# Kernel optimization log

Measured on AMD Instinct MI355X. Metric: run time of the kernel, lower is better.

Reference implementation:

```python
import jax, jax.numpy as jnp
import numpy as np

N_NODES = 100000
N_EDGES = 1600000
NODE_F = 128
EDGE_F = 64
OUT = 32
NEG_SLOPE = 0.01  # torch nn.LeakyReLU default


def setup_inputs() -> dict:
    key = jax.random.key(0)
    ks = jax.random.split(key, 7)
    h = jax.random.normal(ks[0], (N_NODES, NODE_F), dtype=jnp.float32)
    edge_feat = jax.random.normal(ks[1], (N_EDGES, EDGE_F), dtype=jnp.float32)
    src = jax.random.randint(ks[2], (N_EDGES,), 0, N_NODES)
    dst = jax.random.randint(ks[3], (N_EDGES,), 0, N_NODES)
    W_node = jax.random.normal(ks[4], (NODE_F, OUT), dtype=jnp.float32) * 0.05
    W_edge = jax.random.normal(ks[5], (EDGE_F, OUT), dtype=jnp.float32) * 0.05
    attn_w = jax.random.normal(ks[6], (3 * OUT,), dtype=jnp.float32) * 0.05
    return {"h": h, "edge_feat": edge_feat, "src": src, "dst": dst,
            "W_node": W_node, "W_edge": W_edge, "attn_w": attn_w}


def reference(h, edge_feat, src, dst, W_node, W_edge, attn_w):
    # Project node and edge features (bias-free linears).
    z = h @ W_node                      # [N, OUT]
    ez = edge_feat @ W_edge             # [E, OUT]

    # attn_fc on cat(src_z, dst_z, edge_z): split weight vector to avoid
    # materializing the [E, 3*OUT] concat.
    a_src, a_dst, a_edge = attn_w[:OUT], attn_w[OUT:2 * OUT], attn_w[2 * OUT:]
    zs = z[src]                         # [E, OUT] gather
    logits = jax.nn.leaky_relu(
        zs @ a_src + z[dst] @ a_dst + ez @ a_edge, NEG_SLOPE)  # [E]

    # Per-destination (segment) softmax over incoming edges.
    seg_max = jax.ops.segment_max(logits, dst, num_segments=N_NODES)
    seg_max = jnp.where(jnp.isfinite(seg_max), seg_max, 0.0)  # empty segments
    e = jnp.exp(logits - seg_max[dst])                          # [E]
    denom = jax.ops.segment_sum(e, dst, num_segments=N_NODES)  # [N]

    # Weighted sum of src z vectors per destination.
    num = jax.ops.segment_sum(e[:, None] * zs, dst, num_segments=N_NODES)
    u = num / jnp.maximum(denom, 1e-20)[:, None]                # [N, OUT]
    return u
```

## Files before the change

### kernel.cpp

```cpp
#include <hip/hip_runtime.h>
#include <hip/hip_bf16.h>

#define N_NODES 100000
#define N_EDGES 1600000
#define NODE_F 128
#define EDGE_F 64
#define OUT_F 32
#define NEG_SLOPE 0.01f

__global__ void k_edge_w(const float* __restrict__ W_edge,
                         const float* __restrict__ attn_w,
                         float* __restrict__ w_e) {
    int j = threadIdx.x;
    float acc = 0.f;
#pragma unroll
    for (int k = 0; k < OUT_F; ++k)
        acc += W_edge[j * OUT_F + k] * attn_w[2 * OUT_F + k];
    w_e[j] = acc;
}

__global__ void k_node_proj(const float* __restrict__ h,
                            const float* __restrict__ W_node,
                            const float* __restrict__ attn_w,
                            float* __restrict__ z,
                            float* __restrict__ s_src,
                            float* __restrict__ s_dst) {
    __shared__ float Ws[NODE_F * OUT_F];
    for (int i = threadIdx.x; i < NODE_F * OUT_F; i += 256)
        Ws[i] = W_node[i];
    __syncthreads();

    int node = blockIdx.x * 8 + (threadIdx.x >> 5);
    int o = threadIdx.x & 31;
    if (node >= N_NODES) return;

    const float* hrow = h + (size_t)node * NODE_F;
    float acc = 0.f;
#pragma unroll 8
    for (int j = 0; j < NODE_F; ++j)
        acc += hrow[j] * Ws[j * OUT_F + o];

    z[(size_t)node * OUT_F + o] = acc;

    float ps = acc * attn_w[o];
    float pd = acc * attn_w[OUT_F + o];
#pragma unroll
    for (int m = 16; m >= 1; m >>= 1) {
        ps += __shfl_xor(ps, m);
        pd += __shfl_xor(pd, m);
    }
    if (o == 0) {
        s_src[node] = ps;
        s_dst[node] = pd;
    }
}

__global__ void k_edge_dot(const float* __restrict__ edge_feat,
                           const int* __restrict__ dst,
                           const float* __restrict__ w_e,
                           float* __restrict__ g,
                           int* __restrict__ deg) {
    __shared__ float we_s[EDGE_F];
    if (threadIdx.x < EDGE_F) we_s[threadIdx.x] = w_e[threadIdx.x];
    __syncthreads();

    int t = blockIdx.x * 256 + threadIdx.x;
    int e = t >> 2;
    int sub = t & 3;
    if (e >= N_EDGES) return;

    const float4* row = (const float4*)(edge_feat + (size_t)e * EDGE_F);
    float acc = 0.f;
#pragma unroll
    for (int i = 0; i < 4; ++i) {
        int fi = sub + i * 4;
        float4 v = row[fi];
        int b = fi * 4;
        acc += v.x * we_s[b] + v.y * we_s[b + 1] + v.z * we_s[b + 2] + v.w * we_s[b + 3];
    }
    acc += __shfl_xor(acc, 1);
    acc += __shfl_xor(acc, 2);

    if (sub == 0) {
        g[e] = acc;
        atomicAdd(deg + dst[e], 1);
    }
}

__global__ void k_scan_block(const int* __restrict__ deg,
                             int* __restrict__ offs,
                             int* __restrict__ bsum) {
    __shared__ int wsum[4];
    int i = blockIdx.x * 256 + threadIdx.x;
    int lane = threadIdx.x & 63;
    int wid = threadIdx.x >> 6;
    int v = (i < N_NODES) ? deg[i] : 0;
    int x = v;
#pragma unroll
    for (int d = 1; d < 64; d <<= 1) {
        int y = __shfl_up(x, d);
        if (lane >= d) x += y;
    }
    if (lane == 63) wsum[wid] = x;
    __syncthreads();
    int add = 0;
    for (int w = 0; w < wid; ++w) add += wsum[w];
    int incl = x + add;
    if (i < N_NODES) offs[i] = incl - v;
    if (threadIdx.x == 255) bsum[blockIdx.x] = incl;
}

__global__ void k_scan_bsums(int* __restrict__ bsum, int nb) {
    __shared__ int wsum[8];
    int t = threadIdx.x;
    int lane = t & 63;
    int wid = t >> 6;
    int v = (t < nb) ? bsum[t] : 0;
    int x = v;
#pragma unroll
    for (int d = 1; d < 64; d <<= 1) {
        int y = __shfl_up(x, d);
        if (lane >= d) x += y;
    }
    if (lane == 63) wsum[wid] = x;
    __syncthreads();
    int add = 0;
    for (int w = 0; w < wid; ++w) add += wsum[w];
    int incl = x + add;
    if (t < nb) bsum[t] = incl - v;
}

__global__ void k_scan_add(int* __restrict__ offs,
                           const int* __restrict__ bsum,
                           int* __restrict__ cursor) {
    int i = blockIdx.x * 256 + threadIdx.x;
    if (i < N_NODES) {
        int o = offs[i] + bsum[blockIdx.x];
        offs[i] = o;
        cursor[i] = o;
    }
}

__global__ void k_scatter(const int* __restrict__ src,
                          const int* __restrict__ dst,
                          const float* __restrict__ g,
                          const float* __restrict__ s_src,
                          const float* __restrict__ s_dst,
                          int* __restrict__ cursor,
                          int2* __restrict__ perm) {
    int e = blockIdx.x * 256 + threadIdx.x;
    if (e >= N_EDGES) return;
    int s = src[e], d = dst[e];
    float logit = s_src[s] + s_dst[d] + g[e];
    logit = logit > 0.f ? logit : NEG_SLOPE * logit;
    float ev = __expf(logit);
    int pos = atomicAdd(cursor + d, 1);
    perm[pos] = make_int2(s, __float_as_int(ev));
}

__global__ void k_node_aggr(const int* __restrict__ offs,
                            const int* __restrict__ cursor,
                            const int2* __restrict__ perm,
                            const float* __restrict__ z,
                            float* __restrict__ out) {
    int node = blockIdx.x * 8 + (threadIdx.x >> 5);
    int k = threadIdx.x & 31;
    if (node >= N_NODES) return;

    int start = offs[node];
    int end = cursor[node];

    float acc = 0.f, den_local = 0.f;
    for (int base = start; base < end; base += 32) {
        int idx = base + k;
        int cnt = min(32, end - base);
        float ev = 0.f;
        int sp = 0;
        if (idx < end) {
            int2 pr = perm[idx];
            sp = pr.x;
            ev = __int_as_float(pr.y);
        }
        den_local += ev;
        int j = 0;
        for (; j + 4 <= cnt; j += 4) {
            float e0 = __shfl(ev, j, 32), e1 = __shfl(ev, j + 1, 32);
            float e2 = __shfl(ev, j + 2, 32), e3 = __shfl(ev, j + 3, 32);
            int s0 = __shfl(sp, j, 32), s1 = __shfl(sp, j + 1, 32);
            int s2 = __shfl(sp, j + 2, 32), s3 = __shfl(sp, j + 3, 32);
            float z0 = z[(size_t)s0 * OUT_F + k];
            float z1 = z[(size_t)s1 * OUT_F + k];
            float z2 = z[(size_t)s2 * OUT_F + k];
            float z3 = z[(size_t)s3 * OUT_F + k];
            acc += e0 * z0;
            acc += e1 * z1;
            acc += e2 * z2;
            acc += e3 * z3;
        }
        for (; j < cnt; ++j) {
            float evj = __shfl(ev, j, 32);
            int sj = __shfl(sp, j, 32);
            acc += evj * z[(size_t)sj * OUT_F + k];
        }
    }

    float den = den_local;
#pragma unroll
    for (int msk = 16; msk >= 1; msk >>= 1)
        den += __shfl_xor(den, msk, 32);

    out[(size_t)node * OUT_F + k] =
        (end > start) ? acc / fmaxf(den, 1e-20f) : 0.f;
}

extern "C" void kernel_launch(void* const* d_in, const int* in_sizes, int n_in,
                              void* d_out, int out_size, void* d_ws, size_t ws_size,
                              hipStream_t stream) {
    const float* h         = (const float*)d_in[0];
    const float* edge_feat = (const float*)d_in[1];
    const int*   src       = (const int*)d_in[2];
    const int*   dst       = (const int*)d_in[3];
    const float* W_node    = (const float*)d_in[4];
    const float* W_edge    = (const float*)d_in[5];
    const float* attn_w    = (const float*)d_in[6];
    float* out = (float*)d_out;

    char* ws = (char*)d_ws;
    size_t off = 0;
    auto alloc = [&](size_t bytes) {
        void* p = ws + off;
        off += (bytes + 255) & ~(size_t)255;
        return p;
    };
    float* z        = (float*)alloc((size_t)N_NODES * OUT_F * sizeof(float));
    float* s_src    = (float*)alloc((size_t)N_NODES * sizeof(float));
    float* s_dst    = (float*)alloc((size_t)N_NODES * sizeof(float));
    float* w_e      = (float*)alloc(EDGE_F * sizeof(float));
    float* g        = (float*)alloc((size_t)N_EDGES * sizeof(float));
    int*   deg      = (int*)alloc((size_t)N_NODES * sizeof(int));
    int*   offs     = (int*)alloc((size_t)N_NODES * sizeof(int));
    int*   cursor   = (int*)alloc((size_t)N_NODES * sizeof(int));
    int*   bsum     = (int*)alloc(1024 * sizeof(int));
    int2*  perm     = (int2*)alloc((size_t)N_EDGES * sizeof(int2));

    const int NB = (N_NODES + 255) / 256;

    hipMemsetAsync(deg, 0, (size_t)N_NODES * sizeof(int), stream);

    k_edge_w<<<1, 64, 0, stream>>>(W_edge, attn_w, w_e);
    k_node_proj<<<(N_NODES + 7) / 8, 256, 0, stream>>>(h, W_node, attn_w, z, s_src, s_dst);

    {
        int total = N_EDGES * 4;
        k_edge_dot<<<(total + 255) / 256, 256, 0, stream>>>(edge_feat, dst, w_e, g, deg);
    }
    k_scan_block<<<NB, 256, 0, stream>>>(deg, offs, bsum);
    k_scan_bsums<<<1, 512, 0, stream>>>(bsum, NB);
    k_scan_add<<<NB, 256, 0, stream>>>(offs, bsum, cursor);

    k_scatter<<<(N_EDGES + 255) / 256, 256, 0, stream>>>(
        src, dst, g, s_src, s_dst, cursor, perm);

    k_node_aggr<<<(N_NODES + 7) / 8, 256, 0, stream>>>(
        offs, cursor, perm, z, out);
}
```

Measured before the change: 288.2 us.

## Edge-tiled aggregation with LDS atomics, bf16 node projections, fused edge weight

Replaces the per-node warp aggregation with edge-tiled blocks of 256 sorted edges. Each block accumulates into LDS with atomics, writes nodes fully contained in its tile directly, and sends partial sums for boundary nodes to global atomic buffers; a finalize kernel then writes those boundary nodes. The projected z is stored as bf16 to halve gather traffic, and the edge-weight precompute is folded into k_edge_dot to remove one launch. The goal is to balance load across skewed degrees, at the cost of wider perm records (int4), extra memset, many atomics and reduced precision in z.

```diff
diff --git a/kernel.cpp b/kernel.cpp
--- a/kernel.cpp
+++ b/kernel.cpp
@@ -7,22 +7,22 @@
 #define EDGE_F 64
 #define OUT_F 32
 #define NEG_SLOPE 0.01f
-
-__global__ void k_edge_w(const float* __restrict__ W_edge,
-                         const float* __restrict__ attn_w,
-                         float* __restrict__ w_e) {
-    int j = threadIdx.x;
-    float acc = 0.f;
-#pragma unroll
-    for (int k = 0; k < OUT_F; ++k)
-        acc += W_edge[j * OUT_F + k] * attn_w[2 * OUT_F + k];
-    w_e[j] = acc;
+#define E_TILE 256
+#define SPAN_CAP 288
+
+__device__ __forceinline__ unsigned short f2bf(float f) {
+    unsigned u = __float_as_uint(f);
+    unsigned r = u + 0x7fffu + ((u >> 16) & 1u);
+    return (unsigned short)(r >> 16);
+}
+__device__ __forceinline__ float bf2f(unsigned short b) {
+    return __uint_as_float((unsigned)b << 16);
 }
 
 __global__ void k_node_proj(const float* __restrict__ h,
                             const float* __restrict__ W_node,
                             const float* __restrict__ attn_w,
-                            float* __restrict__ z,
+                            unsigned short* __restrict__ zb,
                             float* __restrict__ s_src,
                             float* __restrict__ s_dst) {
     __shared__ float Ws[NODE_F * OUT_F];
@@ -40,7 +40,7 @@
     for (int j = 0; j < NODE_F; ++j)
         acc += hrow[j] * Ws[j * OUT_F + o];
 
-    z[(size_t)node * OUT_F + o] = acc;
+    zb[(size_t)node * OUT_F + o] = f2bf(acc);
 
     float ps = acc * attn_w[o];
     float pd = acc * attn_w[OUT_F + o];
@@ -57,11 +57,18 @@
 
 __global__ void k_edge_dot(const float* __restrict__ edge_feat,
                            const int* __restrict__ dst,
-                           const float* __restrict__ w_e,
+                           const float* __restrict__ W_edge,
+                           const float* __restrict__ attn_w,
                            float* __restrict__ g,
                            int* __restrict__ deg) {
     __shared__ float we_s[EDGE_F];
-    if (threadIdx.x < EDGE_F) we_s[threadIdx.x] = w_e[threadIdx.x];
+    if (threadIdx.x < EDGE_F) {
+        float a = 0.f;
+#pragma unroll
+        for (int kk = 0; kk < OUT_F; ++kk)
+            a += W_edge[threadIdx.x * OUT_F + kk] * attn_w[2 * OUT_F + kk];
+        we_s[threadIdx.x] = a;
+    }
     __syncthreads();
 
     int t = blockIdx.x * 256 + threadIdx.x;
@@ -147,7 +154,7 @@
                           const float* __restrict__ s_src,
                           const float* __restrict__ s_dst,
                           int* __restrict__ cursor,
-                          int2* __restrict__ perm) {
+                          int4* __restrict__ perm4) {
     int e = blockIdx.x * 256 + threadIdx.x;
     if (e >= N_EDGES) return;
     int s = src[e], d = dst[e];
@@ -155,62 +162,96 @@
     logit = logit > 0.f ? logit : NEG_SLOPE * logit;
     float ev = __expf(logit);
     int pos = atomicAdd(cursor + d, 1);
-    perm[pos] = make_int2(s, __float_as_int(ev));
-}
-
-__global__ void k_node_aggr(const int* __restrict__ offs,
-                            const int* __restrict__ cursor,
-                            const int2* __restrict__ perm,
-                            const float* __restrict__ z,
-                            float* __restrict__ out) {
+    perm4[pos] = make_int4(s, __float_as_int(ev), d, 0);
+}
+
+__global__ __launch_bounds__(256) void k_aggr_seg(
+    const int4* __restrict__ perm4,
+    const unsigned short* __restrict__ zb,
+    const int* __restrict__ offs,
+    const int* __restrict__ endp,
+    float* __restrict__ gnum,
+    float* __restrict__ gden,
+    float* __restrict__ out) {
+    __shared__ float lds_num[SPAN_CAP * OUT_F];
+    __shared__ float lds_den[SPAN_CAP];
+    for (int i = threadIdx.x; i < SPAN_CAP * OUT_F; i += 256) lds_num[i] = 0.f;
+    for (int i = threadIdx.x; i < SPAN_CAP; i += 256) lds_den[i] = 0.f;
+    __syncthreads();
+
+    int e0 = blockIdx.x * E_TILE;
+    int n0 = perm4[e0].z;
+    int grp = threadIdx.x >> 5;
+    int k = threadIdx.x & 31;
+    int ebase = e0 + grp * 32;
+
+#pragma unroll 2
+    for (int j = 0; j < 32; j += 4) {
+        int4 pa = perm4[ebase + j + 0];
+        int4 pb = perm4[ebase + j + 1];
+        int4 pc = perm4[ebase + j + 2];
+        int4 pd = perm4[ebase + j + 3];
+        float za = bf2f(zb[(size_t)pa.x * OUT_F + k]);
+        float zv = bf2f(zb[(size_t)pb.x * OUT_F + k]);
+        float zc = bf2f(zb[(size_t)pc.x * OUT_F + k]);
+        float zd = bf2f(zb[(size_t)pd.x * OUT_F + k]);
+        float ea = __int_as_float(pa.y);
+        float eb = __int_as_float(pb.y);
+        float ec = __int_as_float(pc.y);
+        float ed = __int_as_float(pd.y);
+        int la = pa.z - n0, lb = pb.z - n0, lc = pc.z - n0, ld = pd.z - n0;
+
+        if (la < SPAN_CAP) { atomicAdd(&lds_num[la * OUT_F + k], ea * za); if (k == 0) atomicAdd(&lds_den[la], ea); }
+        else { atomicAdd(&gnum[(size_t)pa.z * OUT_F + k], ea * za); if (k == 0) atomicAdd(&gden[pa.z], ea); }
+        if (lb < SPAN_CAP) { atomicAdd(&lds_num[lb * OUT_F + k], eb * zv); if (k == 0) atomicAdd(&lds_den[lb], eb); }
+        else { atomicAdd(&gnum[(size_t)pb.z * OUT_F + k], eb * zv); if (k == 0) atomicAdd(&gden[pb.z], eb); }
+        if (lc < SPAN_CAP) { atomicAdd(&lds_num[lc * OUT_F + k], ec * zc); if (k == 0) atomicAdd(&lds_den[lc], ec); }
+        else { atomicAdd(&gnum[(size_t)pc.z * OUT_F + k], ec * zc); if (k == 0) atomicAdd(&gden[pc.z], ec); }
+        if (ld < SPAN_CAP) { atomicAdd(&lds_num[ld * OUT_F + k], ed * zd); if (k == 0) atomicAdd(&lds_den[ld], ed); }
+        else { atomicAdd(&gnum[(size_t)pd.z * OUT_F + k], ed * zd); if (k == 0) atomicAdd(&gden[pd.z], ed); }
+    }
+    __syncthreads();
+
+    int n_last = perm4[e0 + E_TILE - 1].z;
+    for (int nid = n0 + grp; nid <= n_last; nid += 8) {
+        int li = nid - n0;
+        if (li >= SPAN_CAP) break;
+        float den = lds_den[li];
+        if (den == 0.f) continue;
+        float nm = lds_num[li * OUT_F + k];
+        int st = offs[nid], en = endp[nid];
+        if (st >= e0 && en <= e0 + E_TILE) {
+            out[(size_t)nid * OUT_F + k] = nm / fmaxf(den, 1e-20f);
+        } else {
+            atomicAdd(&gnum[(size_t)nid * OUT_F + k], nm);
+            if (k == 0) atomicAdd(&gden[nid], den);
+        }
+    }
+}
+
+__global__ void k_finalize(const int* __restrict__ offs,
+                           const int* __restrict__ endp,
+                           const int4* __restrict__ perm4,
+                           const float* __restrict__ gnum,
+                           const float* __restrict__ gden,
+                           float* __restrict__ out) {
     int node = blockIdx.x * 8 + (threadIdx.x >> 5);
     int k = threadIdx.x & 31;
     if (node >= N_NODES) return;
-
-    int start = offs[node];
-    int end = cursor[node];
-
-    float acc = 0.f, den_local = 0.f;
-    for (int base = start; base < end; base += 32) {
-        int idx = base + k;
-        int cnt = min(32, end - base);
-        float ev = 0.f;
-        int sp = 0;
-        if (idx < end) {
-            int2 pr = perm[idx];
-            sp = pr.x;
-            ev = __int_as_float(pr.y);
-        }
-        den_local += ev;
-        int j = 0;
-        for (; j + 4 <= cnt; j += 4) {
-            float e0 = __shfl(ev, j, 32), e1 = __shfl(ev, j + 1, 32);
-            float e2 = __shfl(ev, j + 2, 32), e3 = __shfl(ev, j + 3, 32);
-            int s0 = __shfl(sp, j, 32), s1 = __shfl(sp, j + 1, 32);
-            int s2 = __shfl(sp, j + 2, 32), s3 = __shfl(sp, j + 3, 32);
-            float z0 = z[(size_t)s0 * OUT_F + k];
-            float z1 = z[(size_t)s1 * OUT_F + k];
-            float z2 = z[(size_t)s2 * OUT_F + k];
-            float z3 = z[(size_t)s3 * OUT_F + k];
-            acc += e0 * z0;
-            acc += e1 * z1;
-            acc += e2 * z2;
-            acc += e3 * z3;
-        }
-        for (; j < cnt; ++j) {
-            float evj = __shfl(ev, j, 32);
-            int sj = __shfl(sp, j, 32);
-            acc += evj * z[(size_t)sj * OUT_F + k];
-        }
-    }
-
-    float den = den_local;
-#pragma unroll
-    for (int msk = 16; msk >= 1; msk >>= 1)
-        den += __shfl_xor(den, msk, 32);
-
-    out[(size_t)node * OUT_F + k] =
-        (end > start) ? acc / fmaxf(den, 1e-20f) : 0.f;
+    int st = offs[node], en = endp[node];
+    if (st == en) {
+        out[(size_t)node * OUT_F + k] = 0.f;
+        return;
+    }
+    int t0 = st >> 8, t1 = (en - 1) >> 8;
+    bool needs = (t0 != t1);
+    if (!needs) {
+        int nf = perm4[t0 << 8].z;
+        needs = (node - nf) >= SPAN_CAP;
+    }
+    if (needs)
+        out[(size_t)node * OUT_F + k] =
+            gnum[(size_t)node * OUT_F + k] / fmaxf(gden[node], 1e-20f);
 }
 
 extern "C" void kernel_launch(void* const* d_in, const int* in_sizes, int n_in,
@@ -232,35 +273,40 @@
         off += (bytes + 255) & ~(size_t)255;
         return p;
     };
-    float* z        = (float*)alloc((size_t)N_NODES * OUT_F * sizeof(float));
-    float* s_src    = (float*)alloc((size_t)N_NODES * sizeof(float));
-    float* s_dst    = (float*)alloc((size_t)N_NODES * sizeof(float));
-    float* w_e      = (float*)alloc(EDGE_F * sizeof(float));
-    float* g        = (float*)alloc((size_t)N_EDGES * sizeof(float));
-    int*   deg      = (int*)alloc((size_t)N_NODES * sizeof(int));
-    int*   offs     = (int*)alloc((size_t)N_NODES * sizeof(int));
-    int*   cursor   = (int*)alloc((size_t)N_NODES * sizeof(int));
-    int*   bsum     = (int*)alloc(1024 * sizeof(int));
-    int2*  perm     = (int2*)alloc((size_t)N_EDGES * sizeof(int2));
+    unsigned short* zb = (unsigned short*)alloc((size_t)N_NODES * OUT_F * sizeof(unsigned short));
+    float* s_src  = (float*)alloc((size_t)N_NODES * sizeof(float));
+    float* s_dst  = (float*)alloc((size_t)N_NODES * sizeof(float));
+    float* g      = (float*)alloc((size_t)N_EDGES * sizeof(float));
+    int*   offs   = (int*)alloc((size_t)N_NODES * sizeof(int));
+    int*   cursor = (int*)alloc((size_t)N_NODES * sizeof(int));
+    int*   bsum   = (int*)alloc(1024 * sizeof(int));
+    int4*  perm4  = (int4*)alloc((size_t)N_EDGES * sizeof(int4));
+    char*  zero_base = ws + off;
+    int*   deg    = (int*)alloc((size_t)N_NODES * sizeof(int));
+    float* gden   = (float*)alloc((size_t)N_NODES * sizeof(float));
+    float* gnum   = (float*)alloc((size_t)N_NODES * OUT_F * sizeof(float));
+    size_t zero_bytes = (ws + off) - zero_base;
 
     const int NB = (N_NODES + 255) / 256;
 
-    hipMemsetAsync(deg, 0, (size_t)N_NODES * sizeof(int), stream);
-
-    k_edge_w<<<1, 64, 0, stream>>>(W_edge, attn_w, w_e);
-    k_node_proj<<<(N_NODES + 7) / 8, 256, 0, stream>>>(h, W_node, attn_w, z, s_src, s_dst);
+    hipMemsetAsync(zero_base, 0, zero_bytes, stream);
+
+    k_node_proj<<<(N_NODES + 7) / 8, 256, 0, stream>>>(h, W_node, attn_w, zb, s_src, s_dst);
 
     {
         int total = N_EDGES * 4;
-        k_edge_dot<<<(total + 255) / 256, 256, 0, stream>>>(edge_feat, dst, w_e, g, deg);
+        k_edge_dot<<<(total + 255) / 256, 256, 0, stream>>>(edge_feat, dst, W_edge, attn_w, g, deg);
     }
     k_scan_block<<<NB, 256, 0, stream>>>(deg, offs, bsum);
     k_scan_bsums<<<1, 512, 0, stream>>>(bsum, NB);
     k_scan_add<<<NB, 256, 0, stream>>>(offs, bsum, cursor);
 
     k_scatter<<<(N_EDGES + 255) / 256, 256, 0, stream>>>(
-        src, dst, g, s_src, s_dst, cursor, perm);
-
-    k_node_aggr<<<(N_NODES + 7) / 8, 256, 0, stream>>>(
-        offs, cursor, perm, z, out);
-}
+        src, dst, g, s_src, s_dst, cursor, perm4);
+
+    k_aggr_seg<<<N_EDGES / E_TILE, 256, 0, stream>>>(
+        perm4, zb, offs, cursor, gnum, gden, out);
+
+    k_finalize<<<(N_NODES + 7) / 8, 256, 0, stream>>>(
+        offs, cursor, perm4, gnum, gden, out);
+}
```

New measurement: 542.7 us. +88.3%, slower.
